# Kernel optimization log

Hardware: AMD Instinct MI355X
Metric: run time of the kernel (lower is better)

Reference implementation:

```python
import jax, jax.numpy as jnp
import numpy as np
from jax import lax

EPS = 1e-12

def _l2norm(v, axis):
    n = jnp.linalg.norm(v, axis=axis, keepdims=True)
    return v / jnp.maximum(n, EPS)

def setup_inputs() -> dict:
    key = jax.random.key(0)
    k1, k2, k3 = jax.random.split(key, 3)
    C, H, W, K = 512, 192, 192, 64
    x = jax.random.normal(k1, (C, H, W), dtype=jnp.float32)
    conv_w = jax.random.normal(k2, (K, C), dtype=jnp.float32) * 0.05  # 1x1 conv, no bias (vladv2=False)
    centroids = jax.random.uniform(k3, (K, C), dtype=jnp.float32)
    return {"x": x, "conv_w": conv_w, "centroids": centroids}

def reference(x, conv_w, centroids):
    K = conv_w.shape[0]
    x4 = x[None]                      # [1,C,H,W]
    N, C, H, W = x4.shape
    L = H * W
    # descriptor-wise L2 normalization over channels
    x4 = _l2norm(x4, axis=1)
    # 1x1 conv -> soft assignment over clusters
    logits = jnp.einsum('kc,nchw->nkhw', conv_w, x4)
    soft = jax.nn.softmax(logits, axis=1)          # [N,K,H,W]
    sa_flat = soft.reshape(N, K, L)
    # top-2 cluster indices per location (argmax + second largest)
    _, top2 = lax.top_k(sa_flat.transpose(0, 2, 1), 2)  # [N,L,2]
    first, second = top2[..., 0], top2[..., 1]
    # unfold 3x3, padding 1: windows [N, L, K, 9] in (kh,kw) order
    pad = jnp.pad(soft, ((0, 0), (0, 0), (1, 1), (1, 1)))
    patches = jnp.stack([pad[:, :, di:di + H, dj:dj + W]
                         for di in range(3) for dj in range(3)], axis=2)  # [N,K,9,H,W]
    windows = patches.reshape(N, K, 9, L).transpose(0, 3, 1, 2)           # [N,L,K,9]
    # keep only windows of the top-2 clusters at each location
    karange = jnp.arange(K)[None, None, :]
    keep = (karange == first[:, :, None]) | (karange == second[:, :, None])  # [N,L,K]
    wsel = windows * keep[..., None].astype(windows.dtype)
    # fold (transpose of unfold): overlap-add back to [N,K,H,W]
    ws = wsel.transpose(0, 2, 3, 1).reshape(N, K, 9, H, W)
    out_pad = jnp.zeros((N, K, H + 2, W + 2), dtype=ws.dtype)
    t = 0
    for di in range(3):
        for dj in range(3):
            out_pad = out_pad.at[:, :, di:di + H, dj:dj + W].add(ws[:, :, t])
            t += 1
    weight = out_pad[:, :, 1:H + 1, 1:W + 1]
    # border mask: (min distance to border)^4
    ii = jnp.arange(H); jj = jnp.arange(W)
    mi = jnp.minimum(H - 1 - ii, ii)[:, None]
    mj = jnp.minimum(W - 1 - jj, jj)[None, :]
    m = jnp.minimum(mi, mj).astype(weight.dtype)
    m2 = m * m
    mask = m2 * m2
    weight = weight * mask[None, None]
    sa2 = weight.reshape(N, K, L)
    # per-cluster residual accumulation, vectorized (replaces the 64-iter loop)
    xf = x4.reshape(N, C, L)
    vlad = jnp.einsum('nkl,ncl->nkc', sa2, xf) - sa2.sum(-1)[..., None] * centroids[None]
    vlad = _l2norm(vlad, axis=2)               # intra-normalization
    v = vlad.reshape(N, -1)
    v = _l2norm(v, axis=1)
    return v
```

## Files before the change

### kernel.cpp

```cpp
#include <hip/hip_runtime.h>

#define HH 192
#define WW 192
#define LL (HH * WW)
#define CC 512
#define KK 64
#define EPSF 1e-12f
typedef unsigned long long ull;
typedef unsigned int uint;
typedef unsigned short ushort;

#define NCHUNK 192
#define CHUNKL (LL / NCHUNK)

typedef short bf16x8 __attribute__((ext_vector_type(8)));
typedef float f32x4 __attribute__((ext_vector_type(4)));

__device__ inline void split3(float v, ushort& h, ushort& md, ushort& lo) {
    uint b  = __float_as_uint(v);
    uint hb = b & 0xFFFF0000u;
    float r1 = v - __uint_as_float(hb);
    uint mb = __float_as_uint(r1) & 0xFFFF0000u;
    float r2 = r1 - __uint_as_float(mb);
    uint lb = __float_as_uint(r2) & 0xFFFF0000u;
    h = (ushort)(hb >> 16); md = (ushort)(mb >> 16); lo = (ushort)(lb >> 16);
}

__global__ __launch_bounds__(256) void k0_prep(const float* __restrict__ w,
                                               ushort* __restrict__ Whi,
                                               ushort* __restrict__ Wmid,
                                               ushort* __restrict__ Wlo,
                                               float* __restrict__ Szero) {
    int idx = blockIdx.x * 256 + threadIdx.x;
    int k = idx >> 9;
    int c = idx & 511;
    int s = c >> 5, w32 = c & 31, quad = w32 >> 3, j = w32 & 7;
    int kg = k >> 4, m = k & 15;
    int dst = (((s * 4 + kg) * 4 + quad) * 16 + m) * 8 + j;
    float v = w[idx];
    ushort h, md, lo;
    split3(v, h, md, lo);
    Whi[dst] = h; Wmid[dst] = md; Wlo[dst] = lo;
    if (blockIdx.x == 0 && threadIdx.x < 128) Szero[threadIdx.x] = 0.f;
}

__global__ __launch_bounds__(128) void k1_logits(const float* __restrict__ x,
                                                 const ushort* __restrict__ Whi,
                                                 const ushort* __restrict__ Wmid,
                                                 const ushort* __restrict__ Wlo,
                                                 float* __restrict__ soft,
                                                 float* __restrict__ invn,
                                                 ull* __restrict__ keep) {
    int t = threadIdx.x, lane = t & 63, wid = t >> 6;
    int m = lane & 15, quad = lane >> 4;
    int pb = blockIdx.x * 64 + wid * 32;

    f32x4 acc[4][2];
#pragma unroll
    for (int kg = 0; kg < 4; ++kg)
#pragma unroll
        for (int cg = 0; cg < 2; ++cg) acc[kg][cg] = (f32x4){0.f, 0.f, 0.f, 0.f};
    float ssA[2] = {0.f, 0.f};

    const float* xq = x + (size_t)(quad * 8) * LL + pb + m;

    for (int s = 0; s < 16; ++s) {
        bf16x8 Ah[4], Am[4], Al[4];
#pragma unroll
        for (int kg = 0; kg < 4; ++kg) {
            size_t off = (size_t)(((s * 4 + kg) * 64 + lane) * 8);
            Ah[kg] = *(const bf16x8*)(Whi  + off);
            Am[kg] = *(const bf16x8*)(Wmid + off);
            Al[kg] = *(const bf16x8*)(Wlo  + off);
        }
        float xv[2][8];
#pragma unroll
        for (int j = 0; j < 8; ++j) {
            const float* xr = xq + (size_t)j * LL;
            xv[0][j] = xr[0];
            xv[1][j] = xr[16];
        }
        xq += (size_t)32 * LL;
        bf16x8 Bh[2], Bm[2], Bl[2];
#pragma unroll
        for (int cg = 0; cg < 2; ++cg)
#pragma unroll
            for (int j = 0; j < 8; ++j) {
                float v = xv[cg][j];
                ssA[cg] = fmaf(v, v, ssA[cg]);
                ushort h, md, lo;
                split3(v, h, md, lo);
                Bh[cg][j] = (short)h; Bm[cg][j] = (short)md; Bl[cg][j] = (short)lo;
            }
#pragma unroll
        for (int kg = 0; kg < 4; ++kg)
#pragma unroll
            for (int cg = 0; cg < 2; ++cg) {
                f32x4 a = acc[kg][cg];
                a = __builtin_amdgcn_mfma_f32_16x16x32_bf16(Ah[kg], Bh[cg], a, 0, 0, 0);
                a = __builtin_amdgcn_mfma_f32_16x16x32_bf16(Ah[kg], Bm[cg], a, 0, 0, 0);
                a = __builtin_amdgcn_mfma_f32_16x16x32_bf16(Am[kg], Bh[cg], a, 0, 0, 0);
                a = __builtin_amdgcn_mfma_f32_16x16x32_bf16(Ah[kg], Bl[cg], a, 0, 0, 0);
                a = __builtin_amdgcn_mfma_f32_16x16x32_bf16(Al[kg], Bh[cg], a, 0, 0, 0);
                a = __builtin_amdgcn_mfma_f32_16x16x32_bf16(Am[kg], Bm[cg], a, 0, 0, 0);
                acc[kg][cg] = a;
            }
    }

#pragma unroll
    for (int cg = 0; cg < 2; ++cg) {
        float ssv = ssA[cg];
        ssv += __shfl_xor(ssv, 16);
        ssv += __shfl_xor(ssv, 32);
        float iv = 1.0f / fmaxf(sqrtf(ssv), EPSF);
        int px = pb + cg * 16 + m;
        if (quad == 0) invn[px] = iv;

        float lg[16];
        float M1 = -3.0e38f, M2 = -3.0e38f; int I1 = 0, I2 = 0;
#pragma unroll
        for (int kg = 0; kg < 4; ++kg)
#pragma unroll
            for (int r = 0; r < 4; ++r) {
                float v = acc[kg][cg][r] * iv;
                lg[kg * 4 + r] = v;
                int kk = kg * 16 + quad * 4 + r;
                if (v > M1)      { M2 = M1; I2 = I1; M1 = v; I1 = kk; }
                else if (v > M2) { M2 = v; I2 = kk; }
            }
#pragma unroll
        for (int st = 0; st < 2; ++st) {
            int d = 16 << st;
            float a1 = __shfl_xor(M1, d); int b1 = __shfl_xor(I1, d);
            float a2 = __shfl_xor(M2, d); int b2 = __shfl_xor(I2, d);
            if (a1 > M1 || (a1 == M1 && b1 < I1)) { M2 = M1; I2 = I1; M1 = a1; I1 = b1; }
            else if (a1 > M2 || (a1 == M2 && b1 < I2)) { M2 = a1; I2 = b1; }
            if (a2 > M1 || (a2 == M1 && b2 < I1)) { M2 = M1; I2 = I1; M1 = a2; I1 = b2; }
            else if (a2 > M2 || (a2 == M2 && b2 < I2)) { M2 = a2; I2 = b2; }
        }

        float es = 0.f;
#pragma unroll
        for (int q = 0; q < 16; ++q) { float e = __expf(lg[q] - M1); lg[q] = e; es += e; }
        es += __shfl_xor(es, 16);
        es += __shfl_xor(es, 32);
        float rs = 1.0f / es;

        float4* sp = (float4*)(soft + (size_t)px * KK + quad * 4);
#pragma unroll
        for (int kg = 0; kg < 4; ++kg) {
            float4 o;
            o.x = lg[kg * 4 + 0] * rs; o.y = lg[kg * 4 + 1] * rs;
            o.z = lg[kg * 4 + 2] * rs; o.w = lg[kg * 4 + 3] * rs;
            sp[kg * 4] = o;
        }
        if (quad == 0) keep[px] = (1ull << I1) | (1ull << I2);
    }
}

__global__ __launch_bounds__(256) void k2_weight(float* __restrict__ soft,
                                                 const ull* __restrict__ keep,
                                                 const float* __restrict__ invn,
                                                 float* __restrict__ S) {
    __shared__ float sred[4][64];
    int t = threadIdx.x, lane = t & 63, wid = t >> 6;
    int l0 = blockIdx.x * 32 + wid * 8;
    float sk = 0.f;
#pragma unroll
    for (int p = 0; p < 8; ++p) {
        int l = l0 + p;
        int i = l / WW, j = l % WW;
        int m = min(min(i, HH - 1 - i), min(j, WW - 1 - j));
        float bm = (float)m; bm *= bm; bm *= bm;
        int cnt = 0;
#pragma unroll
        for (int di = -1; di <= 1; ++di) {
            int ii = i + di;
            if (ii < 0 || ii >= HH) continue;
#pragma unroll
            for (int dj = -1; dj <= 1; ++dj) {
                int jj = j + dj;
                if (jj < 0 || jj >= WW) continue;
                ull nb = keep[ii * WW + jj];
                cnt += (int)((nb >> lane) & 1ull);
            }
        }
        float v = soft[(size_t)l * KK + lane];
        float u = v * (float)cnt * bm;
        sk += u;
        soft[(size_t)l * KK + lane] = u * invn[l];
    }
    sred[wid][lane] = sk;
    __syncthreads();
    if (wid == 0)
        atomicAdd(&S[lane], sred[0][lane] + sred[1][lane] + sred[2][lane] + sred[3][lane]);
}

__device__ inline void cvt_pair(float v0, float v1, uint& hp, uint& lp) {
    uint b0 = __float_as_uint(v0), b1 = __float_as_uint(v1);
    uint h0 = b0 & 0xFFFF0000u, h1 = b1 & 0xFFFF0000u;
    float r0 = v0 - __uint_as_float(h0);
    float r1 = v1 - __uint_as_float(h1);
    hp = (h0 >> 16) | h1;
    lp = (__float_as_uint(r0) >> 16) | (__float_as_uint(r1) & 0xFFFF0000u);
}

__global__ __launch_bounds__(256) void k3_mfma(const float* __restrict__ w2,
                                               const float* __restrict__ x,
                                               float* __restrict__ partials) {
    __shared__ ushort wa_hi[64][40], wa_lo[64][40];
    __shared__ ushort xb_hi[128][40], xb_lo[128][40];
    int chunk = blockIdx.x;
    int c0 = blockIdx.y * 128;
    int l0 = chunk * CHUNKL;
    int t = threadIdx.x, lane = t & 63, wid = t >> 6;
    int m = lane & 15, quad = lane >> 4;

    f32x4 acc[4][2];
#pragma unroll
    for (int kg = 0; kg < 4; ++kg)
#pragma unroll
        for (int cg = 0; cg < 2; ++cg) acc[kg][cg] = (f32x4){0.f, 0.f, 0.f, 0.f};

    for (int lb = 0; lb < CHUNKL; lb += 32) {
        {
            int k = t & 63, rg = t >> 6;
#pragma unroll
            for (int i = 0; i < 4; ++i) {
                int lp = rg + 4 * i;
                int gl = l0 + lb + 2 * lp;
                float v0 = w2[(size_t)gl * KK + k];
                float v1 = w2[(size_t)(gl + 1) * KK + k];
                uint hp, lq;
                cvt_pair(v0, v1, hp, lq);
                *(uint*)&wa_hi[k][2 * lp] = hp;
                *(uint*)&wa_lo[k][2 * lp] = lq;
            }
        }
        {
            int lp = t & 15, cb = t >> 4;
            int gl = l0 + lb + 2 * lp;
#pragma unroll
            for (int i = 0; i < 8; ++i) {
                int c = cb + 16 * i;
                float v0 = x[(size_t)(c0 + c) * LL + gl];
                float v1 = x[(size_t)(c0 + c) * LL + gl + 1];
                uint hp, lq;
                cvt_pair(v0, v1, hp, lq);
                *(uint*)&xb_hi[c][2 * lp] = hp;
                *(uint*)&xb_lo[c][2 * lp] = lq;
            }
        }
        __syncthreads();
        bf16x8 Ah[4], Al[4];
#pragma unroll
        for (int kg = 0; kg < 4; ++kg) {
            Ah[kg] = *(bf16x8*)&wa_hi[kg * 16 + m][quad * 8];
            Al[kg] = *(bf16x8*)&wa_lo[kg * 16 + m][quad * 8];
        }
#pragma unroll
        for (int cg = 0; cg < 2; ++cg) {
            int crow = wid * 32 + cg * 16 + m;
            bf16x8 Bh = *(bf16x8*)&xb_hi[crow][quad * 8];
            bf16x8 Bl = *(bf16x8*)&xb_lo[crow][quad * 8];
#pragma unroll
            for (int kg = 0; kg < 4; ++kg) {
                acc[kg][cg] = __builtin_amdgcn_mfma_f32_16x16x32_bf16(Ah[kg], Bh, acc[kg][cg], 0, 0, 0);
                acc[kg][cg] = __builtin_amdgcn_mfma_f32_16x16x32_bf16(Ah[kg], Bl, acc[kg][cg], 0, 0, 0);
                acc[kg][cg] = __builtin_amdgcn_mfma_f32_16x16x32_bf16(Al[kg], Bh, acc[kg][cg], 0, 0, 0);
            }
        }
        __syncthreads();
    }
    float* pp = partials + (size_t)chunk * KK * CC;
#pragma unroll
    for (int kg = 0; kg < 4; ++kg)
#pragma unroll
        for (int cg = 0; cg < 2; ++cg) {
            int cout = c0 + wid * 32 + cg * 16 + m;
#pragma unroll
            for (int r = 0; r < 4; ++r) {
                int kout = kg * 16 + quad * 4 + r;
                pp[(size_t)kout * CC + cout] = acc[kg][cg][r];
            }
        }
}

__global__ __launch_bounds__(512) void k4a_reduce(const float* __restrict__ partials,
                                                  const float* __restrict__ S,
                                                  const float* __restrict__ cent,
                                                  float* __restrict__ vlad,
                                                  float* __restrict__ rowsq) {
    __shared__ float red[512];
    int k = blockIdx.x;
    int ci = threadIdx.x & 127;
    int c = blockIdx.y * 128 + ci;
    int q = threadIdx.x >> 7;
    const float* pk = partials + (size_t)q * (NCHUNK / 4) * KK * CC + (size_t)k * CC + c;
    float s0 = 0.f, s1 = 0.f, s2 = 0.f, s3 = 0.f;
    for (int ch = 0; ch < NCHUNK / 4; ch += 4) {
        s0 += pk[(size_t)(ch + 0) * KK * CC];
        s1 += pk[(size_t)(ch + 1) * KK * CC];
        s2 += pk[(size_t)(ch + 2) * KK * CC];
        s3 += pk[(size_t)(ch + 3) * KK * CC];
    }
    red[threadIdx.x] = (s0 + s1) + (s2 + s3);
    __syncthreads();
    float vsq = 0.f;
    if (q == 0) {
        float v = red[ci] + red[ci + 128] + red[ci + 256] + red[ci + 384];
        v -= S[k] * cent[k * CC + c];
        vlad[k * CC + c] = v;
        vsq = v * v;
    }
    __syncthreads();
    red[threadIdx.x] = vsq;
    __syncthreads();
    for (int off = 256; off > 0; off >>= 1) {
        if (threadIdx.x < off) red[threadIdx.x] += red[threadIdx.x + off];
        __syncthreads();
    }
    if (threadIdx.x == 0) atomicAdd(&rowsq[k], red[0]);
}

__global__ __launch_bounds__(256) void k4c_finish(const float* __restrict__ vlad,
                                                  const float* __restrict__ rowsq,
                                                  float* __restrict__ out) {
    __shared__ float rns[64];
    int t = threadIdx.x;
    if (t < 64) {
        float tot = rowsq[t];
        float r = 1.0f / fmaxf(sqrtf(tot), EPSF);
        float contrib = tot * r * r;
#pragma unroll
        for (int off = 32; off; off >>= 1) contrib += __shfl_xor(contrib, off, 64);
        float ginv = 1.0f / fmaxf(sqrtf(contrib), EPSF);
        rns[t] = r * ginv;
    }
    __syncthreads();
    int idx4 = blockIdx.x * 256 + t;
    int k = idx4 >> 7;
    float s = rns[k];
    float4 v = ((const float4*)vlad)[idx4];
    v.x *= s; v.y *= s; v.z *= s; v.w *= s;
    ((float4*)out)[idx4] = v;
}

extern "C" void kernel_launch(void* const* d_in, const int* in_sizes, int n_in,
                              void* d_out, int out_size, void* d_ws, size_t ws_size,
                              hipStream_t stream) {
    const float* x      = (const float*)d_in[0];
    const float* conv_w = (const float*)d_in[1];
    const float* cent   = (const float*)d_in[2];
    float* out = (float*)d_out;

    float* ws    = (float*)d_ws;
    ushort* Whi  = (ushort*)ws;
    ushort* Wmid = Whi + 32768;
    ushort* Wlo  = Wmid + 32768;
    float* soft  = ws + 49152;
    float* invn  = soft + (size_t)KK * LL;
    float* S     = invn + LL;
    float* rowsq = S + KK;
    float* vlad  = rowsq + KK;
    ull*   keep  = (ull*)(vlad + 32768);
    float* partials = (float*)(keep + LL);

    k0_prep<<<(KK * CC) / 256, 256, 0, stream>>>(conv_w, Whi, Wmid, Wlo, S);
    k1_logits<<<LL / 64, 128, 0, stream>>>(x, Whi, Wmid, Wlo, soft, invn, keep);
    k2_weight<<<LL / 32, 256, 0, stream>>>(soft, keep, invn, S);
    k3_mfma<<<dim3(NCHUNK, 4), 256, 0, stream>>>(soft, x, partials);
    k4a_reduce<<<dim3(KK, 4), 512, 0, stream>>>(partials, S, cent, vlad, rowsq);
    k4c_finish<<<(KK * CC / 4) / 256, 256, 0, stream>>>(vlad, rowsq, out);
}
```

Measured before the change: 203.0 us.

## Split channel reduction across two waves in logits kernel and prefetch x

```diff
diff --git a/kernel.cpp b/kernel.cpp
--- a/kernel.cpp
+++ b/kernel.cpp
@@ -51,9 +51,11 @@
                                                  float* __restrict__ soft,
                                                  float* __restrict__ invn,
                                                  ull* __restrict__ keep) {
+    __shared__ float accL[32][64];
+    __shared__ float ssL[2][64];
     int t = threadIdx.x, lane = t & 63, wid = t >> 6;
     int m = lane & 15, quad = lane >> 4;
-    int pb = blockIdx.x * 64 + wid * 32;
+    int pb = blockIdx.x * 32;
 
     f32x4 acc[4][2];
 #pragma unroll
@@ -62,25 +64,36 @@
         for (int cg = 0; cg < 2; ++cg) acc[kg][cg] = (f32x4){0.f, 0.f, 0.f, 0.f};
     float ssA[2] = {0.f, 0.f};
 
-    const float* xq = x + (size_t)(quad * 8) * LL + pb + m;
-
-    for (int s = 0; s < 16; ++s) {
+    const float* xq = x + (size_t)(wid * 256 + quad * 8) * LL + pb + m;
+
+    float xv[2][8];
+#pragma unroll
+    for (int j = 0; j < 8; ++j) {
+        const float* xr = xq + (size_t)j * LL;
+        xv[0][j] = xr[0];
+        xv[1][j] = xr[16];
+    }
+
+    for (int s = 0; s < 8; ++s) {
+        int s16 = wid * 8 + s;
         bf16x8 Ah[4], Am[4], Al[4];
 #pragma unroll
         for (int kg = 0; kg < 4; ++kg) {
-            size_t off = (size_t)(((s * 4 + kg) * 64 + lane) * 8);
+            size_t off = (size_t)(((s16 * 4 + kg) * 64 + lane) * 8);
             Ah[kg] = *(const bf16x8*)(Whi  + off);
             Am[kg] = *(const bf16x8*)(Wmid + off);
             Al[kg] = *(const bf16x8*)(Wlo  + off);
         }
-        float xv[2][8];
-#pragma unroll
-        for (int j = 0; j < 8; ++j) {
-            const float* xr = xq + (size_t)j * LL;
-            xv[0][j] = xr[0];
-            xv[1][j] = xr[16];
-        }
-        xq += (size_t)32 * LL;
+        float xn[2][8];
+        if (s < 7) {
+            const float* xq2 = xq + (size_t)32 * LL;
+#pragma unroll
+            for (int j = 0; j < 8; ++j) {
+                const float* xr = xq2 + (size_t)j * LL;
+                xn[0][j] = xr[0];
+                xn[1][j] = xr[16];
+            }
+        }
         bf16x8 Bh[2], Bm[2], Bl[2];
 #pragma unroll
         for (int cg = 0; cg < 2; ++cg)
@@ -105,7 +118,37 @@
                 a = __builtin_amdgcn_mfma_f32_16x16x32_bf16(Am[kg], Bm[cg], a, 0, 0, 0);
                 acc[kg][cg] = a;
             }
-    }
+        if (s < 7) {
+#pragma unroll
+            for (int cg = 0; cg < 2; ++cg)
+#pragma unroll
+                for (int j = 0; j < 8; ++j) xv[cg][j] = xn[cg][j];
+            xq += (size_t)32 * LL;
+        }
+    }
+
+    if (wid == 1) {
+#pragma unroll
+        for (int kg = 0; kg < 4; ++kg)
+#pragma unroll
+            for (int cg = 0; cg < 2; ++cg)
+#pragma unroll
+                for (int r = 0; r < 4; ++r)
+                    accL[kg * 8 + cg * 4 + r][lane] = acc[kg][cg][r];
+        ssL[0][lane] = ssA[0];
+        ssL[1][lane] = ssA[1];
+    }
+    __syncthreads();
+    if (wid != 0) return;
+#pragma unroll
+    for (int kg = 0; kg < 4; ++kg)
+#pragma unroll
+        for (int cg = 0; cg < 2; ++cg)
+#pragma unroll
+            for (int r = 0; r < 4; ++r)
+                acc[kg][cg][r] += accL[kg * 8 + cg * 4 + r][lane];
+    ssA[0] += ssL[0][lane];
+    ssA[1] += ssL[1][lane];
 
 #pragma unroll
     for (int cg = 0; cg < 2; ++cg) {
@@ -367,7 +410,7 @@
     float* partials = (float*)(keep + LL);
 
     k0_prep<<<(KK * CC) / 256, 256, 0, stream>>>(conv_w, Whi, Wmid, Wlo, S);
-    k1_logits<<<LL / 64, 128, 0, stream>>>(x, Whi, Wmid, Wlo, soft, invn, keep);
+    k1_logits<<<LL / 32, 128, 0, stream>>>(x, Whi, Wmid, Wlo, soft, invn, keep);
     k2_weight<<<LL / 32, 256, 0, stream>>>(soft, keep, invn, S);
     k3_mfma<<<dim3(NCHUNK, 4), 256, 0, stream>>>(soft, x, partials);
     k4a_reduce<<<dim3(KK, 4), 512, 0, stream>>>(partials, S, cent, vlad, rowsq);
```

Measured after the change: 196.3 us. -3.3%, faster.
